# Kernel tuning notes

Measured on AMD Instinct MI355X. Metric: run time of the kernel, lower is better.

Reference implementation:

```python
import jax, jax.numpy as jnp
import numpy as np


def _forward(x, conv_w, conv_b, lin_w, lin_b, W_in, conv1d_w, conv1d_b, W_x, W_dt, b_dt, A_log, Dp, W_out, We, be, Wa, ba, Wq, bq):
    B, _, H, Wd = x.shape
    E = conv_w.shape[0]
    # conv stem: Conv2d(k=3, pad=1) -> flatten(2) -> Linear(H*W -> img_size)
    z = jax.lax.conv_general_dilated(x, conv_w, (1, 1), [(1, 1), (1, 1)],
                                     dimension_numbers=('NCHW', 'OIHW', 'NCHW'))
    z = z + conv_b[None, :, None, None]
    z = z.reshape(B, E, H * Wd)                              # [B,E,HW]
    z = jnp.einsum('ben,mn->bem', z, lin_w) + lin_b          # [B,E,L]
    u = z.transpose(2, 0, 1)                                 # [L,B,E]: Mamba sees batch=L, seq=B
    # ---- Mamba block (mamba_ssm reference math) ----
    di = W_in.shape[0] // 2
    xz = u @ W_in.T                                          # [L,seq,2*di]
    xm, zg = xz[..., :di], xz[..., di:]
    K = conv1d_w.shape[-1]
    xc = jax.lax.conv_general_dilated(xm.transpose(0, 2, 1), conv1d_w, (1,), [(K - 1, 0)],
                                      dimension_numbers=('NCH', 'OIH', 'NCH'),
                                      feature_group_count=di)  # causal depthwise conv
    xs = jax.nn.silu((xc + conv1d_b[None, :, None]).transpose(0, 2, 1))  # [L,seq,di]
    dbl = xs @ W_x.T                                         # [L,seq,dt_rank+2S]
    dt_rank = W_dt.shape[1]
    S = A_log.shape[1]
    delta = jax.nn.softplus(dbl[..., :dt_rank] @ W_dt.T + b_dt)          # [L,seq,di]
    Bm = dbl[..., dt_rank:dt_rank + S]                       # [L,seq,S]
    Cm = dbl[..., dt_rank + S:]                              # [L,seq,S]
    A = -jnp.exp(A_log)                                      # [di,S]

    def step(h, t):
        d_t, b_t, c_t, x_t = t                               # [L,di],[L,S],[L,S],[L,di]
        h = jnp.exp(d_t[:, :, None] * A) * h + (d_t * x_t)[:, :, None] * b_t[:, None, :]
        return h, jnp.einsum('lds,ls->ld', h, c_t)

    h0 = jnp.zeros((u.shape[0], di, S), xs.dtype)
    _, ys = jax.lax.scan(step, h0, (delta.transpose(1, 0, 2), Bm.transpose(1, 0, 2),
                                    Cm.transpose(1, 0, 2), xs.transpose(1, 0, 2)))
    y = (ys.transpose(1, 0, 2) + xs * Dp) * jax.nn.silu(zg)  # [L,seq,di]
    out = y @ W_out.T                                        # [L,seq,E]
    feat = out[-1]                                           # [B,E] (last 'mamba batch' row)
    return feat @ We.T + be, feat @ Wa.T + ba, feat @ Wq.T + bq


def setup_inputs() -> dict:
    key = jax.random.key(0)
    ks = jax.random.split(key, 16)
    B, C, IMG, E, S, K = 512, 1, 32, 128, 256, 4
    di, dt_rank = 2 * E, 8
    sc = 0.02
    return {
        'x': jax.random.normal(ks[0], (B, C, IMG, IMG), jnp.float32),
        'conv_w': sc * jax.random.normal(ks[1], (E, C, 3, 3), jnp.float32),
        'conv_b': jnp.zeros((E,), jnp.float32),
        'lin_w': sc * jax.random.normal(ks[2], (IMG, IMG * IMG), jnp.float32),
        'lin_b': jnp.zeros((IMG,), jnp.float32),
        'W_in': sc * jax.random.normal(ks[3], (2 * di, E), jnp.float32),
        'conv1d_w': sc * jax.random.normal(ks[4], (di, 1, K), jnp.float32),
        'conv1d_b': jnp.zeros((di,), jnp.float32),
        'W_x': sc * jax.random.normal(ks[5], (dt_rank + 2 * S, di), jnp.float32),
        'W_dt': sc * jax.random.normal(ks[6], (di, dt_rank), jnp.float32),
        'b_dt': 0.1 * jax.random.normal(ks[7], (di,), jnp.float32),
        'A_log': jnp.log(jnp.broadcast_to(jnp.arange(1, S + 1, dtype=jnp.float32), (di, S))),
        'Dp': jnp.ones((di,), jnp.float32),
        'W_out': sc * jax.random.normal(ks[8], (E, di), jnp.float32),
        'We': sc * jax.random.normal(ks[9], (1, E), jnp.float32),
        'be': jnp.zeros((1,), jnp.float32),
        'Wa': sc * jax.random.normal(ks[10], (3, E), jnp.float32),
        'ba': jnp.zeros((3,), jnp.float32),
        'Wq': sc * jax.random.normal(ks[11], (4, E), jnp.float32),
        'bq': jnp.zeros((4,), jnp.float32),
    }


def reference(x, conv_w, conv_b, lin_w, lin_b, W_in, conv1d_w, conv1d_b, W_x, W_dt, b_dt, A_log, Dp, W_out, We, be, Wa, ba, Wq, bq):
    return _forward(x, conv_w, conv_b, lin_w, lin_b, W_in, conv1d_w, conv1d_b, W_x,
                    W_dt, b_dt, A_log, Dp, W_out, We, be, Wa, ba, Wq, bq)
```

## Files before the change

### kernel.cpp

```cpp
#include <hip/hip_runtime.h>
#include <math.h>

#define BATCH 512
#define E     128
#define DI    256
#define S     256
#define DTR   8
#define KCONV 4
#define JWX   520

__device__ __forceinline__ float silu_f(float v) {
    return v / (1.0f + __expf(-v));
}

__global__ __launch_bounds__(256) void kA_pre(
    const float* __restrict__ x, const float* __restrict__ conv_w,
    const float* __restrict__ conv_b, const float* __restrict__ lin_w,
    const float* __restrict__ lin_b, const float* __restrict__ W_in,
    const float* __restrict__ W_x, const float* __restrict__ W_out,
    float* __restrict__ xm, float* __restrict__ zg,
    float* __restrict__ W_xT, float* __restrict__ W_outT)
{
    const int tid = threadIdx.x;
    if (blockIdx.x >= 512) {
        const int bid = blockIdx.x - 512;
        const float* src; float* dst; int J, K, j0;
        if (bid < 9) { src = W_x;   dst = W_xT;   J = JWX; K = DI; j0 = bid * 64; }
        else         { src = W_out; dst = W_outT; J = E;   K = DI; j0 = (bid - 9) * 64; }
        const int j = j0 + (tid & 63);
        if (j >= J) return;
        for (int c = tid >> 6; c < K; c += 4)
            dst[c * J + j] = src[j * K + c];
        return;
    }

    const int b = blockIdx.x;
    __shared__ float lw[1024];
    __shared__ float red[10][4];
    __shared__ float Tsh[10];
    __shared__ float u[E];

    const float4 lv = ((const float4*)(lin_w + 31 * 1024))[tid];
    ((float4*)lw)[tid] = lv;
    __syncthreads();

    float acc[10];
#pragma unroll
    for (int k = 0; k < 10; k++) acc[k] = 0.0f;

    const float4 xv = ((const float4*)(x + (size_t)b * 1024))[tid];
    const int p0 = tid * 4;
    const int h = p0 >> 5, w0 = p0 & 31;
    const float xa[4] = {xv.x, xv.y, xv.z, xv.w};
#pragma unroll
    for (int k = 0; k < 4; k++) {
        const float xval = xa[k];
        const int w = w0 + k;
#pragma unroll
        for (int i = 0; i < 3; i++) {
            const int hh = h - (i - 1);
            if (hh < 0 || hh > 31) continue;
#pragma unroll
            for (int j = 0; j < 3; j++) {
                const int ww = w - (j - 1);
                if (ww < 0 || ww > 31) continue;
                acc[i * 3 + j] += xval * lw[hh * 32 + ww];
            }
        }
    }
    acc[9] = lv.x + lv.y + lv.z + lv.w;

    const int wv = tid >> 6, ln = tid & 63;
#pragma unroll
    for (int k = 0; k < 10; k++) {
#pragma unroll
        for (int m = 1; m < 64; m <<= 1) acc[k] += __shfl_xor(acc[k], m, 64);
    }
    if (ln == 0) {
#pragma unroll
        for (int k = 0; k < 10; k++) red[k][wv] = acc[k];
    }
    __syncthreads();
    if (tid < 10) Tsh[tid] = red[tid][0] + red[tid][1] + red[tid][2] + red[tid][3];
    __syncthreads();

    if (tid < E) {
        const int e = tid;
        float v = lin_b[31] + conv_b[e] * Tsh[9];
#pragma unroll
        for (int k = 0; k < 9; k++) v += conv_w[e * 9 + k] * Tsh[k];
        u[e] = v;
    }
    __syncthreads();

    {
        const float4* w0p = (const float4*)(W_in + (size_t)tid * E);
        const float4* w1p = (const float4*)(W_in + (size_t)(tid + 256) * E);
        float a0 = 0.0f;
#pragma unroll 8
        for (int e4 = 0; e4 < E / 4; e4++) {
            const float4 w = w0p[e4];
            a0 += u[4*e4]*w.x + u[4*e4+1]*w.y + u[4*e4+2]*w.z + u[4*e4+3]*w.w;
        }
        float a1 = 0.0f;
#pragma unroll 8
        for (int e4 = 0; e4 < E / 4; e4++) {
            const float4 w = w1p[e4];
            a1 += u[4*e4]*w.x + u[4*e4+1]*w.y + u[4*e4+2]*w.z + u[4*e4+3]*w.w;
        }
        xm[b * DI + tid] = a0;
        zg[b * DI + tid] = a1;
    }
}

__global__ __launch_bounds__(256) void k2b_conv_wx(
    const float* __restrict__ xm, const float* __restrict__ c1w,
    const float* __restrict__ conv1d_b, const float* __restrict__ W_xT,
    const float* __restrict__ W_dt, const float* __restrict__ b_dt,
    float* __restrict__ xs_g, float* __restrict__ delta_g,
    float* __restrict__ Bm, float* __restrict__ Cm)
{
    const int bb = blockIdx.x * 4;
    const int g = blockIdx.y;
    const int tid = threadIdx.x;
    __shared__ float xs[4][DI];
    __shared__ float dtin[4][8];

    for (int idx = tid; idx < 4 * DI; idx += 256) {
        const int r = idx >> 8, c = idx & 255;
        const int b = bb + r;
        const float4 wc = ((const float4*)c1w)[c];
        float a = conv1d_b[c];
        if (b >= 3) a += xm[(b - 3) * DI + c] * wc.x;
        if (b >= 2) a += xm[(b - 2) * DI + c] * wc.y;
        if (b >= 1) a += xm[(b - 1) * DI + c] * wc.z;
        a += xm[b * DI + c] * wc.w;
        const float s = silu_f(a);
        xs[r][c] = s;
        if (g == 0) xs_g[b * DI + c] = s;
    }
    __syncthreads();

    const int r = tid >> 6;
    const int j = g * 64 + (tid & 63);
    if (j < JWX) {
        float a = 0.0f;
#pragma unroll 8
        for (int c = 0; c < DI; c++) a += xs[r][c] * W_xT[c * JWX + j];
        const int b = bb + r;
        if (j < DTR)          dtin[r][j] = a;
        else if (j < DTR + S) Bm[b * S + (j - DTR)] = a;
        else                  Cm[b * S + (j - DTR - S)] = a;
    }
    __syncthreads();

    if (g == 0) {
        const int d = tid;
        const float bd = b_dt[d];
        const float4 wd0 = ((const float4*)(W_dt + d * DTR))[0];
        const float4 wd1 = ((const float4*)(W_dt + d * DTR))[1];
#pragma unroll
        for (int r2 = 0; r2 < 4; r2++) {
            float a = bd
                + dtin[r2][0]*wd0.x + dtin[r2][1]*wd0.y + dtin[r2][2]*wd0.z + dtin[r2][3]*wd0.w
                + dtin[r2][4]*wd1.x + dtin[r2][5]*wd1.y + dtin[r2][6]*wd1.z + dtin[r2][7]*wd1.w;
            const float sp = (a > 20.0f) ? a : log1pf(__expf(a));
            delta_g[(bb + r2) * DI + d] = sp;
        }
    }
}

template <int NCv>
__global__ __launch_bounds__(256) void k3u_up(
    const float* __restrict__ A_log, const float* __restrict__ delta,
    const float* __restrict__ xs, const float* __restrict__ Bm,
    float* __restrict__ hloc, float* __restrict__ Dchunk)
{
    constexpr int TCv = BATCH / NCv;
    const int tid = threadIdx.x;
    const int wv = tid >> 6, ln = tid & 63;
    const int d = blockIdx.x * 4 + wv;
    const int c = blockIdx.y;
    const int s0 = ln * 4;
    const int t0 = c * TCv;

    const float4 al = *(const float4*)(A_log + d * S + s0);
    float4 A;
    A.x = -__expf(al.x); A.y = -__expf(al.y);
    A.z = -__expf(al.z); A.w = -__expf(al.w);

    float4 h = make_float4(0.f, 0.f, 0.f, 0.f);
    float cd = 0.0f;

    for (int tb = 0; tb < TCv; tb += 8) {
#pragma unroll
        for (int i = 0; i < 8; i++) {
            const int tt = t0 + tb + i;
            const float dd = delta[tt * DI + d];
            cd += dd;
            const float u = dd * xs[tt * DI + d];
            const float4 B = *(const float4*)(Bm + tt * S + s0);
            h.x = __expf(dd * A.x) * h.x + u * B.x;
            h.y = __expf(dd * A.y) * h.y + u * B.y;
            h.z = __expf(dd * A.z) * h.z + u * B.z;
            h.w = __expf(dd * A.w) * h.w + u * B.w;
        }
    }

    *(float4*)(hloc + ((size_t)(c * DI + d)) * S + s0) = h;
    if (ln == 0) Dchunk[c * DI + d] = cd;
}

template <int NCv>
__global__ __launch_bounds__(256) void k3d_down(
    const float* __restrict__ A_log, const float* __restrict__ delta,
    const float* __restrict__ xs, const float* __restrict__ Bm,
    const float* __restrict__ Cm, const float* __restrict__ hloc,
    const float* __restrict__ Dchunk, float* __restrict__ y)
{
    constexpr int TCv = BATCH / NCv;
    const int tid = threadIdx.x;
    const int wv = tid >> 6, ln = tid & 63;
    const int d = blockIdx.x * 4 + wv;
    const int c = (NCv - 1) - blockIdx.y;
    const int s0 = ln * 4;
    const int t0 = c * TCv;

    const float4 al = *(const float4*)(A_log + d * S + s0);
    float4 A;
    A.x = -__expf(al.x); A.y = -__expf(al.y);
    A.z = -__expf(al.z); A.w = -__expf(al.w);

    float4 h = make_float4(0.f, 0.f, 0.f, 0.f);
    for (int cp = 1; cp <= c; cp++) {
        const float4 hl = *(const float4*)(hloc + ((size_t)((cp - 1) * DI + d)) * S + s0);
        const float Dc = Dchunk[(cp - 1) * DI + d];
        h.x = hl.x + __expf(A.x * Dc) * h.x;
        h.y = hl.y + __expf(A.y * Dc) * h.y;
        h.z = hl.z + __expf(A.z * Dc) * h.z;
        h.w = hl.w + __expf(A.w * Dc) * h.w;
    }

    float pr[8];
    for (int tb = 0; tb < TCv; tb += 8) {
#pragma unroll
        for (int i = 0; i < 8; i++) {
            const int tt = t0 + tb + i;
            const float dd = delta[tt * DI + d];
            const float u = dd * xs[tt * DI + d];
            const float4 B = *(const float4*)(Bm + tt * S + s0);
            const float4 C = *(const float4*)(Cm + tt * S + s0);
            h.x = __expf(dd * A.x) * h.x + u * B.x;
            h.y = __expf(dd * A.y) * h.y + u * B.y;
            h.z = __expf(dd * A.z) * h.z + u * B.z;
            h.w = __expf(dd * A.w) * h.w + u * B.w;
            pr[i] = h.x * C.x + h.y * C.y + h.z * C.z + h.w * C.w;
        }
#pragma unroll
        for (int i = 0; i < 8; i++) {
#pragma unroll
            for (int m = 1; m < 64; m <<= 1) pr[i] += __shfl_xor(pr[i], m, 64);
        }
        if (ln == 0) {
#pragma unroll
            for (int i = 0; i < 8; i++) y[(t0 + tb + i) * DI + d] = pr[i];
        }
    }
}

__global__ __launch_bounds__(256) void k4_heads(
    const float* __restrict__ y, const float* __restrict__ xs,
    const float* __restrict__ Dp, const float* __restrict__ zg,
    const float* __restrict__ W_outT,
    const float* __restrict__ We, const float* __restrict__ be,
    const float* __restrict__ Wa, const float* __restrict__ ba,
    const float* __restrict__ Wq, const float* __restrict__ bq,
    float* __restrict__ out)
{
    const int bb = blockIdx.x * 2;
    const int tid = threadIdx.x;
    __shared__ float yf[2][DI];
    __shared__ float feat[2][E];

    for (int idx = tid; idx < 2 * DI; idx += 256) {
        const int r = idx >> 8, c = idx & 255;
        const int b = bb + r;
        const float z = zg[b * DI + c];
        yf[r][c] = (y[b * DI + c] + xs[b * DI + c] * Dp[c]) * silu_f(z);
    }
    __syncthreads();

    {
        const int r = tid >> 7, e = tid & 127;
        float a = 0.0f;
#pragma unroll 8
        for (int dd = 0; dd < DI; dd++) a += yf[r][dd] * W_outT[dd * E + e];
        feat[r][e] = a;
    }
    __syncthreads();

    if (tid < 16) {
        const int r = tid >> 3, hd = tid & 7;
        const int b = bb + r;
        const float* wrow;
        float bias;
        int dst;
        if (hd == 0)      { wrow = We;                 bias = be[0];      dst = b; }
        else if (hd < 4)  { wrow = Wa + (hd - 1) * E;  bias = ba[hd - 1]; dst = 512 + b * 3 + (hd - 1); }
        else              { wrow = Wq + (hd - 4) * E;  bias = bq[hd - 4]; dst = 2048 + b * 4 + (hd - 4); }
        float a = bias;
#pragma unroll 4
        for (int e = 0; e < E; e++) a += feat[r][e] * wrow[e];
        out[dst] = a;
    }
}

template <int NCv>
static void launch_scan(const float* A_log, const float* delta, const float* xs,
                        const float* Bm, const float* Cm, float* y,
                        float* hloc, float* Dchunk, hipStream_t stream)
{
    k3u_up<NCv><<<dim3(64, NCv), 256, 0, stream>>>(A_log, delta, xs, Bm, hloc, Dchunk);
    k3d_down<NCv><<<dim3(64, NCv), 256, 0, stream>>>(A_log, delta, xs, Bm, Cm, hloc, Dchunk, y);
}

extern "C" void kernel_launch(void* const* d_in, const int* in_sizes, int n_in,
                              void* d_out, int out_size, void* d_ws, size_t ws_size,
                              hipStream_t stream)
{
    const float* x        = (const float*)d_in[0];
    const float* conv_w   = (const float*)d_in[1];
    const float* conv_b   = (const float*)d_in[2];
    const float* lin_w    = (const float*)d_in[3];
    const float* lin_b    = (const float*)d_in[4];
    const float* W_in     = (const float*)d_in[5];
    const float* conv1d_w = (const float*)d_in[6];
    const float* conv1d_b = (const float*)d_in[7];
    const float* W_x      = (const float*)d_in[8];
    const float* W_dt     = (const float*)d_in[9];
    const float* b_dt     = (const float*)d_in[10];
    const float* A_log    = (const float*)d_in[11];
    const float* Dp       = (const float*)d_in[12];
    const float* W_out    = (const float*)d_in[13];
    const float* We       = (const float*)d_in[14];
    const float* be       = (const float*)d_in[15];
    const float* Wa       = (const float*)d_in[16];
    const float* ba       = (const float*)d_in[17];
    const float* Wq       = (const float*)d_in[18];
    const float* bq       = (const float*)d_in[19];
    float* out = (float*)d_out;

    float* ws = (float*)d_ws;
    float* xm     = ws;
    float* zg     = xm     + 512 * 256;
    float* xs     = zg     + 512 * 256;
    float* delta  = xs     + 512 * 256;
    float* Bm     = delta  + 512 * 256;
    float* Cm     = Bm     + 512 * 256;
    float* y      = Cm     + 512 * 256;
    float* W_xT   = y      + 512 * 256;
    float* W_outT = W_xT   + 256 * JWX;
    float* tail   = W_outT + 256 * 128;

    const size_t base_floats = (size_t)(tail - ws);
    const size_t avail = ws_size / 4 - base_floats;

    kA_pre<<<523, 256, 0, stream>>>(x, conv_w, conv_b, lin_w, lin_b,
                                    W_in, W_x, W_out,
                                    xm, zg, W_xT, W_outT);
    k2b_conv_wx<<<dim3(128, 9), 256, 0, stream>>>(xm, conv1d_w, conv1d_b, W_xT, W_dt, b_dt,
                                                  xs, delta, Bm, Cm);

    if (avail >= (size_t)32 * DI * S + 32 * DI) {
        float* hloc = tail;
        float* Dch  = hloc + (size_t)32 * DI * S;
        launch_scan<32>(A_log, delta, xs, Bm, Cm, y, hloc, Dch, stream);
    } else if (avail >= (size_t)16 * DI * S + 16 * DI) {
        float* hloc = tail;
        float* Dch  = hloc + (size_t)16 * DI * S;
        launch_scan<16>(A_log, delta, xs, Bm, Cm, y, hloc, Dch, stream);
    } else {
        float* hloc = tail;
        float* Dch  = hloc + (size_t)8 * DI * S;
        launch_scan<8>(A_log, delta, xs, Bm, Cm, y, hloc, Dch, stream);
    }

    k4_heads<<<256, 256, 0, stream>>>(y, xs, Dp, zg, W_outT, We, be, Wa, ba, Wq, bq, out);
}
```

Baseline: 184.5 us.

## Fuse all stages into one persistent kernel with software grid barriers

Replaces the five separate launches (pre-projection, conv+W_x, chunked scan up-sweep, down-sweep, output heads) with one persistent 512-block kernel. The stages are separated by an atomic-counter grid barrier, and a small init kernel resets the barrier state. The goal is to remove per-launch overhead and the idle gaps between dependent kernels. In exchange it relies on all 512 blocks being co-resident (two per CU via launch bounds), which risks deadlock if occupancy drops. It also adds barrier spin latency and fixes the scan chunk count at 32.

```diff
diff --git a/kernel.cpp b/kernel.cpp
--- a/kernel.cpp
+++ b/kernel.cpp
@@ -8,9 +8,326 @@
 #define DTR   8
 #define KCONV 4
 #define JWX   520
+#define NC    32
+#define TCV   (BATCH / NC)
+#define NBLK  512
 
 __device__ __forceinline__ float silu_f(float v) {
     return v / (1.0f + __expf(-v));
+}
+
+__device__ __forceinline__ void gridbar(int* cnt, int* gen) {
+    __syncthreads();
+    if (threadIdx.x == 0) {
+        __threadfence();
+        const int g = __hip_atomic_load(gen, __ATOMIC_RELAXED, __HIP_MEMORY_SCOPE_AGENT);
+        const int arrived =
+            __hip_atomic_fetch_add(cnt, 1, __ATOMIC_ACQ_REL, __HIP_MEMORY_SCOPE_AGENT) + 1;
+        if (arrived == NBLK) {
+            __hip_atomic_store(cnt, 0, __ATOMIC_RELAXED, __HIP_MEMORY_SCOPE_AGENT);
+            __hip_atomic_store(gen, g + 1, __ATOMIC_RELEASE, __HIP_MEMORY_SCOPE_AGENT);
+        } else {
+            while (__hip_atomic_load(gen, __ATOMIC_ACQUIRE, __HIP_MEMORY_SCOPE_AGENT) == g)
+                __builtin_amdgcn_s_sleep(4);
+        }
+        __threadfence();
+    }
+    __syncthreads();
+}
+
+__global__ void kinit(int* cnt, int* gen) {
+    if (threadIdx.x == 0) { *cnt = 0; *gen = 0; }
+}
+
+__global__ __launch_bounds__(256, 2) void mega(
+    const float* __restrict__ x, const float* __restrict__ conv_w,
+    const float* __restrict__ conv_b, const float* __restrict__ lin_w,
+    const float* __restrict__ lin_b, const float* __restrict__ W_in,
+    const float* __restrict__ c1w, const float* __restrict__ conv1d_b,
+    const float* __restrict__ W_x, const float* __restrict__ W_dt,
+    const float* __restrict__ b_dt, const float* __restrict__ A_log,
+    const float* __restrict__ Dp, const float* __restrict__ W_out,
+    const float* __restrict__ We, const float* __restrict__ be,
+    const float* __restrict__ Wa, const float* __restrict__ ba,
+    const float* __restrict__ Wq, const float* __restrict__ bq,
+    float* __restrict__ out,
+    float* __restrict__ xm, float* __restrict__ zg,
+    float* __restrict__ xs_g, float* __restrict__ delta_g,
+    float* __restrict__ Bm, float* __restrict__ Cm,
+    float* __restrict__ y,
+    float* __restrict__ W_xT, float* __restrict__ W_outT,
+    float* __restrict__ hloc, float* __restrict__ Dchunk,
+    int* __restrict__ bcnt, int* __restrict__ bgen)
+{
+    const int tid  = threadIdx.x;
+    const int bid  = blockIdx.x;
+    const int wv = tid >> 6, ln = tid & 63;
+
+    __shared__ float lw[1024];
+    __shared__ float red[10][4];
+    __shared__ float Tsh[10];
+    __shared__ float ush[E];
+    __shared__ float xs_sh[4][DI];
+    __shared__ float dtin[4][8];
+    __shared__ float yf[2][DI];
+    __shared__ float feat[2][E];
+
+    for (int v = bid; v < 523; v += NBLK) {
+        if (v >= 512) {
+            const int t = v - 512;
+            const float* src; float* dst; int J, K, j0;
+            if (t < 9) { src = W_x;   dst = W_xT;   J = JWX; K = DI; j0 = t * 64; }
+            else       { src = W_out; dst = W_outT; J = E;   K = DI; j0 = (t - 9) * 64; }
+            const int j = j0 + ln;
+            if (j < J) {
+                for (int c = wv; c < K; c += 4)
+                    dst[c * J + j] = src[j * K + c];
+            }
+        } else {
+            const int b = v;
+            const float4 lv = ((const float4*)(lin_w + 31 * 1024))[tid];
+            ((float4*)lw)[tid] = lv;
+            __syncthreads();
+
+            float acc[10];
+#pragma unroll
+            for (int k = 0; k < 10; k++) acc[k] = 0.0f;
+
+            const float4 xv = ((const float4*)(x + (size_t)b * 1024))[tid];
+            const int p0 = tid * 4;
+            const int h = p0 >> 5, w0 = p0 & 31;
+            const float xa[4] = {xv.x, xv.y, xv.z, xv.w};
+#pragma unroll
+            for (int k = 0; k < 4; k++) {
+                const float xval = xa[k];
+                const int w = w0 + k;
+#pragma unroll
+                for (int i = 0; i < 3; i++) {
+                    const int hh = h - (i - 1);
+                    if (hh < 0 || hh > 31) continue;
+#pragma unroll
+                    for (int j = 0; j < 3; j++) {
+                        const int ww = w - (j - 1);
+                        if (ww < 0 || ww > 31) continue;
+                        acc[i * 3 + j] += xval * lw[hh * 32 + ww];
+                    }
+                }
+            }
+            acc[9] = lv.x + lv.y + lv.z + lv.w;
+
+#pragma unroll
+            for (int k = 0; k < 10; k++) {
+#pragma unroll
+                for (int m = 1; m < 64; m <<= 1) acc[k] += __shfl_xor(acc[k], m, 64);
+            }
+            if (ln == 0) {
+#pragma unroll
+                for (int k = 0; k < 10; k++) red[k][wv] = acc[k];
+            }
+            __syncthreads();
+            if (tid < 10) Tsh[tid] = red[tid][0] + red[tid][1] + red[tid][2] + red[tid][3];
+            __syncthreads();
+
+            if (tid < E) {
+                const int e = tid;
+                float val = lin_b[31] + conv_b[e] * Tsh[9];
+#pragma unroll
+                for (int k = 0; k < 9; k++) val += conv_w[e * 9 + k] * Tsh[k];
+                ush[e] = val;
+            }
+            __syncthreads();
+
+            {
+                const float4* w0p = (const float4*)(W_in + (size_t)tid * E);
+                const float4* w1p = (const float4*)(W_in + (size_t)(tid + 256) * E);
+                float a0 = 0.0f;
+#pragma unroll 8
+                for (int e4 = 0; e4 < E / 4; e4++) {
+                    const float4 w = w0p[e4];
+                    a0 += ush[4*e4]*w.x + ush[4*e4+1]*w.y + ush[4*e4+2]*w.z + ush[4*e4+3]*w.w;
+                }
+                float a1 = 0.0f;
+#pragma unroll 8
+                for (int e4 = 0; e4 < E / 4; e4++) {
+                    const float4 w = w1p[e4];
+                    a1 += ush[4*e4]*w.x + ush[4*e4+1]*w.y + ush[4*e4+2]*w.z + ush[4*e4+3]*w.w;
+                }
+                xm[b * DI + tid] = a0;
+                zg[b * DI + tid] = a1;
+            }
+            __syncthreads();
+        }
+    }
+
+    gridbar(bcnt, bgen);
+
+    for (int v = bid; v < 128 * 9; v += NBLK) {
+        const int g  = v >> 7;
+        const int bb = (v & 127) * 4;
+
+        for (int idx = tid; idx < 4 * DI; idx += 256) {
+            const int r = idx >> 8, c = idx & 255;
+            const int b = bb + r;
+            const float4 wc = ((const float4*)c1w)[c];
+            float a = conv1d_b[c];
+            if (b >= 3) a += xm[(b - 3) * DI + c] * wc.x;
+            if (b >= 2) a += xm[(b - 2) * DI + c] * wc.y;
+            if (b >= 1) a += xm[(b - 1) * DI + c] * wc.z;
+            a += xm[b * DI + c] * wc.w;
+            const float s = silu_f(a);
+            xs_sh[r][c] = s;
+            if (g == 0) xs_g[b * DI + c] = s;
+        }
+        __syncthreads();
+
+        const int r = tid >> 6;
+        const int j = g * 64 + ln;
+        if (j < JWX) {
+            float a = 0.0f;
+#pragma unroll 8
+            for (int c = 0; c < DI; c++) a += xs_sh[r][c] * W_xT[c * JWX + j];
+            const int b = bb + r;
+            if (j < DTR)          dtin[r][j] = a;
+            else if (j < DTR + S) Bm[b * S + (j - DTR)] = a;
+            else                  Cm[b * S + (j - DTR - S)] = a;
+        }
+        __syncthreads();
+
+        if (g == 0) {
+            const int d = tid;
+            const float bd = b_dt[d];
+            const float4 wd0 = ((const float4*)(W_dt + d * DTR))[0];
+            const float4 wd1 = ((const float4*)(W_dt + d * DTR))[1];
+#pragma unroll
+            for (int r2 = 0; r2 < 4; r2++) {
+                float a = bd
+                    + dtin[r2][0]*wd0.x + dtin[r2][1]*wd0.y + dtin[r2][2]*wd0.z + dtin[r2][3]*wd0.w
+                    + dtin[r2][4]*wd1.x + dtin[r2][5]*wd1.y + dtin[r2][6]*wd1.z + dtin[r2][7]*wd1.w;
+                delta_g[(bb + r2) * DI + d] = (a > 20.0f) ? a : log1pf(__expf(a));
+            }
+        }
+        __syncthreads();
+    }
+
+    gridbar(bcnt, bgen);
+
+    for (int v = bid; v < 64 * NC; v += NBLK) {
+        const int xp = v & 63, c = v >> 6;
+        const int d = xp * 4 + wv;
+        const int s0 = ln * 4;
+        const int t0 = c * TCV;
+
+        const float4 al = *(const float4*)(A_log + d * S + s0);
+        float4 A;
+        A.x = -__expf(al.x); A.y = -__expf(al.y);
+        A.z = -__expf(al.z); A.w = -__expf(al.w);
+
+        float4 h = make_float4(0.f, 0.f, 0.f, 0.f);
+        float cd = 0.0f;
+        for (int tb = 0; tb < TCV; tb += 8) {
+#pragma unroll
+            for (int i = 0; i < 8; i++) {
+                const int tt = t0 + tb + i;
+                const float dd = delta_g[tt * DI + d];
+                cd += dd;
+                const float u = dd * xs_g[tt * DI + d];
+                const float4 B = *(const float4*)(Bm + tt * S + s0);
+                h.x = __expf(dd * A.x) * h.x + u * B.x;
+                h.y = __expf(dd * A.y) * h.y + u * B.y;
+                h.z = __expf(dd * A.z) * h.z + u * B.z;
+                h.w = __expf(dd * A.w) * h.w + u * B.w;
+            }
+        }
+        *(float4*)(hloc + ((size_t)(c * DI + d)) * S + s0) = h;
+        if (ln == 0) Dchunk[c * DI + d] = cd;
+    }
+
+    gridbar(bcnt, bgen);
+
+    for (int v = bid; v < 64 * NC; v += NBLK) {
+        const int xp = v & 63;
+        const int c = (NC - 1) - (v >> 6);
+        const int d = xp * 4 + wv;
+        const int s0 = ln * 4;
+        const int t0 = c * TCV;
+
+        const float4 al = *(const float4*)(A_log + d * S + s0);
+        float4 A;
+        A.x = -__expf(al.x); A.y = -__expf(al.y);
+        A.z = -__expf(al.z); A.w = -__expf(al.w);
+
+        float4 h = make_float4(0.f, 0.f, 0.f, 0.f);
+        for (int cp = 1; cp <= c; cp++) {
+            const float4 hl = *(const float4*)(hloc + ((size_t)((cp - 1) * DI + d)) * S + s0);
+            const float Dc = Dchunk[(cp - 1) * DI + d];
+            h.x = hl.x + __expf(A.x * Dc) * h.x;
+            h.y = hl.y + __expf(A.y * Dc) * h.y;
+            h.z = hl.z + __expf(A.z * Dc) * h.z;
+            h.w = hl.w + __expf(A.w * Dc) * h.w;
+        }
+
+        float pr[8];
+        for (int tb = 0; tb < TCV; tb += 8) {
+#pragma unroll
+            for (int i = 0; i < 8; i++) {
+                const int tt = t0 + tb + i;
+                const float dd = delta_g[tt * DI + d];
+                const float u = dd * xs_g[tt * DI + d];
+                const float4 B = *(const float4*)(Bm + tt * S + s0);
+                const float4 C = *(const float4*)(Cm + tt * S + s0);
+                h.x = __expf(dd * A.x) * h.x + u * B.x;
+                h.y = __expf(dd * A.y) * h.y + u * B.y;
+                h.z = __expf(dd * A.z) * h.z + u * B.z;
+                h.w = __expf(dd * A.w) * h.w + u * B.w;
+                pr[i] = h.x * C.x + h.y * C.y + h.z * C.z + h.w * C.w;
+            }
+#pragma unroll
+            for (int i = 0; i < 8; i++) {
+#pragma unroll
+                for (int m = 1; m < 64; m <<= 1) pr[i] += __shfl_xor(pr[i], m, 64);
+            }
+            if (ln == 0) {
+#pragma unroll
+                for (int i = 0; i < 8; i++) y[(t0 + tb + i) * DI + d] = pr[i];
+            }
+        }
+    }
+
+    gridbar(bcnt, bgen);
+
+    for (int v = bid; v < 256; v += NBLK) {
+        const int bb = v * 2;
+        for (int idx = tid; idx < 2 * DI; idx += 256) {
+            const int r = idx >> 8, cc = idx & 255;
+            const int b = bb + r;
+            const float z = zg[b * DI + cc];
+            yf[r][cc] = (y[b * DI + cc] + xs_g[b * DI + cc] * Dp[cc]) * silu_f(z);
+        }
+        __syncthreads();
+        {
+            const int r = tid >> 7, e = tid & 127;
+            float a = 0.0f;
+#pragma unroll 8
+            for (int dd = 0; dd < DI; dd++) a += yf[r][dd] * W_outT[dd * E + e];
+            feat[r][e] = a;
+        }
+        __syncthreads();
+        if (tid < 16) {
+            const int r = tid >> 3, hd = tid & 7;
+            const int b = bb + r;
+            const float* wrow;
+            float bias;
+            int dst;
+            if (hd == 0)      { wrow = We;                 bias = be[0];      dst = b; }
+            else if (hd < 4)  { wrow = Wa + (hd - 1) * E;  bias = ba[hd - 1]; dst = 512 + b * 3 + (hd - 1); }
+            else              { wrow = Wq + (hd - 4) * E;  bias = bq[hd - 4]; dst = 2048 + b * 4 + (hd - 4); }
+            float a = bias;
+#pragma unroll 4
+            for (int e = 0; e < E; e++) a += feat[r][e] * wrow[e];
+            out[dst] = a;
+        }
+        __syncthreads();
+    }
 }
 
 __global__ __launch_bounds__(256) void kA_pre(
@@ -170,19 +487,17 @@
     }
 }
 
-template <int NCv>
 __global__ __launch_bounds__(256) void k3u_up(
     const float* __restrict__ A_log, const float* __restrict__ delta,
     const float* __restrict__ xs, const float* __restrict__ Bm,
     float* __restrict__ hloc, float* __restrict__ Dchunk)
 {
-    constexpr int TCv = BATCH / NCv;
     const int tid = threadIdx.x;
     const int wv = tid >> 6, ln = tid & 63;
     const int d = blockIdx.x * 4 + wv;
     const int c = blockIdx.y;
     const int s0 = ln * 4;
-    const int t0 = c * TCv;
+    const int t0 = c * TCV;
 
     const float4 al = *(const float4*)(A_log + d * S + s0);
     float4 A;
@@ -191,8 +506,7 @@
 
     float4 h = make_float4(0.f, 0.f, 0.f, 0.f);
     float cd = 0.0f;
-
-    for (int tb = 0; tb < TCv; tb += 8) {
+    for (int tb = 0; tb < TCV; tb += 8) {
 #pragma unroll
         for (int i = 0; i < 8; i++) {
             const int tt = t0 + tb + i;
@@ -206,25 +520,22 @@
             h.w = __expf(dd * A.w) * h.w + u * B.w;
         }
     }
-
     *(float4*)(hloc + ((size_t)(c * DI + d)) * S + s0) = h;
     if (ln == 0) Dchunk[c * DI + d] = cd;
 }
 
-template <int NCv>
 __global__ __launch_bounds__(256) void k3d_down(
     const float* __restrict__ A_log, const float* __restrict__ delta,
     const float* __restrict__ xs, const float* __restrict__ Bm,
     const float* __restrict__ Cm, const float* __restrict__ hloc,
     const float* __restrict__ Dchunk, float* __restrict__ y)
 {
-    constexpr int TCv = BATCH / NCv;
     const int tid = threadIdx.x;
     const int wv = tid >> 6, ln = tid & 63;
     const int d = blockIdx.x * 4 + wv;
-    const int c = (NCv - 1) - blockIdx.y;
+    const int c = (NC - 1) - blockIdx.y;
     const int s0 = ln * 4;
-    const int t0 = c * TCv;
+    const int t0 = c * TCV;
 
     const float4 al = *(const float4*)(A_log + d * S + s0);
     float4 A;
@@ -242,7 +553,7 @@
     }
 
     float pr[8];
-    for (int tb = 0; tb < TCv; tb += 8) {
+    for (int tb = 0; tb < TCV; tb += 8) {
 #pragma unroll
         for (int i = 0; i < 8; i++) {
             const int tt = t0 + tb + i;
@@ -313,15 +624,6 @@
         for (int e = 0; e < E; e++) a += feat[r][e] * wrow[e];
         out[dst] = a;
     }
-}
-
-template <int NCv>
-static void launch_scan(const float* A_log, const float* delta, const float* xs,
-                        const float* Bm, const float* Cm, float* y,
-                        float* hloc, float* Dchunk, hipStream_t stream)
-{
-    k3u_up<NCv><<<dim3(64, NCv), 256, 0, stream>>>(A_log, delta, xs, Bm, hloc, Dchunk);
-    k3d_down<NCv><<<dim3(64, NCv), 256, 0, stream>>>(A_log, delta, xs, Bm, Cm, hloc, Dchunk, y);
 }
 
 extern "C" void kernel_launch(void* const* d_in, const int* in_sizes, int n_in,
@@ -360,30 +662,29 @@
     float* y      = Cm     + 512 * 256;
     float* W_xT   = y      + 512 * 256;
     float* W_outT = W_xT   + 256 * JWX;
-    float* tail   = W_outT + 256 * 128;
-
-    const size_t base_floats = (size_t)(tail - ws);
-    const size_t avail = ws_size / 4 - base_floats;
-
-    kA_pre<<<523, 256, 0, stream>>>(x, conv_w, conv_b, lin_w, lin_b,
-                                    W_in, W_x, W_out,
-                                    xm, zg, W_xT, W_outT);
-    k2b_conv_wx<<<dim3(128, 9), 256, 0, stream>>>(xm, conv1d_w, conv1d_b, W_xT, W_dt, b_dt,
-                                                  xs, delta, Bm, Cm);
-
-    if (avail >= (size_t)32 * DI * S + 32 * DI) {
-        float* hloc = tail;
-        float* Dch  = hloc + (size_t)32 * DI * S;
-        launch_scan<32>(A_log, delta, xs, Bm, Cm, y, hloc, Dch, stream);
-    } else if (avail >= (size_t)16 * DI * S + 16 * DI) {
-        float* hloc = tail;
-        float* Dch  = hloc + (size_t)16 * DI * S;
-        launch_scan<16>(A_log, delta, xs, Bm, Cm, y, hloc, Dch, stream);
+    float* hloc   = W_outT + 256 * 128;
+    float* Dchunk = hloc   + (size_t)NC * DI * S;
+    int*   bstate = (int*)(Dchunk + NC * DI);
+
+    const size_t need_floats = (size_t)(Dchunk + NC * DI + 16 - ws);
+    if (ws_size / 4 >= need_floats) {
+        int* bcnt = bstate;
+        int* bgen = bstate + 1;
+        kinit<<<1, 64, 0, stream>>>(bcnt, bgen);
+        mega<<<NBLK, 256, 0, stream>>>(
+            x, conv_w, conv_b, lin_w, lin_b, W_in,
+            conv1d_w, conv1d_b, W_x, W_dt, b_dt, A_log, Dp, W_out,
+            We, be, Wa, ba, Wq, bq, out,
+            xm, zg, xs, delta, Bm, Cm, y, W_xT, W_outT, hloc, Dchunk,
+            bcnt, bgen);
     } else {
-        float* hloc = tail;
-        float* Dch  = hloc + (size_t)8 * DI * S;
-        launch_scan<8>(A_log, delta, xs, Bm, Cm, y, hloc, Dch, stream);
-    }
-
-    k4_heads<<<256, 256, 0, stream>>>(y, xs, Dp, zg, W_outT, We, be, Wa, ba, Wq, bq, out);
-}
+        kA_pre<<<523, 256, 0, stream>>>(x, conv_w, conv_b, lin_w, lin_b,
+                                        W_in, W_x, W_out, xm, zg, W_xT, W_outT);
+        k2b_conv_wx<<<dim3(128, 9), 256, 0, stream>>>(xm, conv1d_w, conv1d_b, W_xT,
+                                                      W_dt, b_dt, xs, delta, Bm, Cm);
+        k3u_up<<<dim3(64, NC), 256, 0, stream>>>(A_log, delta, xs, Bm, hloc, Dchunk);
+        k3d_down<<<dim3(64, NC), 256, 0, stream>>>(A_log, delta, xs, Bm, Cm,
+                                                   hloc, Dchunk, y);
+        k4_heads<<<256, 256, 0, stream>>>(y, xs, Dp, zg, W_outT, We, be, Wa, ba, Wq, bq, out);
+    }
+}
```

Measured after the change: 668.0 us. 3.62x slower.

## Fuse pipeline into one persistent kernel with flag-based inter-block synchronization

Applied to the files above, without the earlier changes.

Replaces the five separate launches (preprocessing, conv+W_x projection, scan up-sweep, scan down-sweep, heads) with a single 512-block persistent kernel. Blocks coordinate through global sentinel flags and counters, so each scan chunk starts as soon as its input rows are ready and the heads run per chunk as soon as its outputs are done. It also drops the weight-transpose pass and recomputes the three preceding in_proj rows per block for the causal conv, so xm never goes to global memory. The scheme relies on all 512 blocks being resident at once to avoid deadlock, and the extra recomputation adds redundant work.

```diff
diff --git a/kernel.cpp b/kernel.cpp
--- a/kernel.cpp
+++ b/kernel.cpp
@@ -8,320 +8,342 @@
 #define DTR   8
 #define KCONV 4
 #define JWX   520
+#define NC    32
+#define TCV   (BATCH / NC)
+#define NBLK  512
+#define SENT  0x7C3A91E5
 
 __device__ __forceinline__ float silu_f(float v) {
     return v / (1.0f + __expf(-v));
 }
 
-__global__ __launch_bounds__(256) void kA_pre(
+__device__ __forceinline__ int ld_flag(const int* p) {
+    return __hip_atomic_load(p, __ATOMIC_RELAXED, __HIP_MEMORY_SCOPE_AGENT);
+}
+__device__ __forceinline__ void st_flag(int* p, int v) {
+    __hip_atomic_store(p, v, __ATOMIC_RELAXED, __HIP_MEMORY_SCOPE_AGENT);
+}
+__device__ __forceinline__ void acq_fence() {
+    __builtin_amdgcn_fence(__ATOMIC_ACQUIRE, "agent");
+}
+
+__device__ __forceinline__ float dot128(const float* __restrict__ w,
+                                        const float* __restrict__ u) {
+    const float4* wp = (const float4*)w;
+    float a = 0.0f;
+#pragma unroll 8
+    for (int e4 = 0; e4 < 32; e4++) {
+        const float4 ww = wp[e4];
+        a += u[4*e4]*ww.x + u[4*e4+1]*ww.y + u[4*e4+2]*ww.z + u[4*e4+3]*ww.w;
+    }
+    return a;
+}
+
+__global__ __launch_bounds__(256, 2) void mega(
     const float* __restrict__ x, const float* __restrict__ conv_w,
     const float* __restrict__ conv_b, const float* __restrict__ lin_w,
     const float* __restrict__ lin_b, const float* __restrict__ W_in,
-    const float* __restrict__ W_x, const float* __restrict__ W_out,
-    float* __restrict__ xm, float* __restrict__ zg,
-    float* __restrict__ W_xT, float* __restrict__ W_outT)
+    const float* __restrict__ c1w, const float* __restrict__ conv1d_b,
+    const float* __restrict__ W_x, const float* __restrict__ W_dt,
+    const float* __restrict__ b_dt, const float* __restrict__ A_log,
+    const float* __restrict__ Dp, const float* __restrict__ W_out,
+    const float* __restrict__ We, const float* __restrict__ be,
+    const float* __restrict__ Wa, const float* __restrict__ ba,
+    const float* __restrict__ Wq, const float* __restrict__ bq,
+    float* __restrict__ out,
+    float* __restrict__ zg, float* __restrict__ xs_g,
+    float* __restrict__ delta_g, float* __restrict__ Bm,
+    float* __restrict__ Cm, float* __restrict__ y,
+    float* __restrict__ hloc, float* __restrict__ Dchunk,
+    int* __restrict__ rowflag, int* __restrict__ upflag,
+    int* __restrict__ donecnt)
 {
     const int tid = threadIdx.x;
-    if (blockIdx.x >= 512) {
-        const int bid = blockIdx.x - 512;
-        const float* src; float* dst; int J, K, j0;
-        if (bid < 9) { src = W_x;   dst = W_xT;   J = JWX; K = DI; j0 = bid * 64; }
-        else         { src = W_out; dst = W_outT; J = E;   K = DI; j0 = (bid - 9) * 64; }
-        const int j = j0 + (tid & 63);
-        if (j >= J) return;
-        for (int c = tid >> 6; c < K; c += 4)
-            dst[c * J + j] = src[j * K + c];
-        return;
-    }
-
-    const int b = blockIdx.x;
+    const int bid = blockIdx.x;
+    const int wv = tid >> 6, ln = tid & 63;
+
     __shared__ float lw[1024];
     __shared__ float red[10][4];
     __shared__ float Tsh[10];
-    __shared__ float u[E];
-
-    const float4 lv = ((const float4*)(lin_w + 31 * 1024))[tid];
-    ((float4*)lw)[tid] = lv;
-    __syncthreads();
-
-    float acc[10];
-#pragma unroll
-    for (int k = 0; k < 10; k++) acc[k] = 0.0f;
-
-    const float4 xv = ((const float4*)(x + (size_t)b * 1024))[tid];
-    const int p0 = tid * 4;
-    const int h = p0 >> 5, w0 = p0 & 31;
-    const float xa[4] = {xv.x, xv.y, xv.z, xv.w};
-#pragma unroll
-    for (int k = 0; k < 4; k++) {
-        const float xval = xa[k];
-        const int w = w0 + k;
-#pragma unroll
-        for (int i = 0; i < 3; i++) {
-            const int hh = h - (i - 1);
-            if (hh < 0 || hh > 31) continue;
-#pragma unroll
-            for (int j = 0; j < 3; j++) {
-                const int ww = w - (j - 1);
-                if (ww < 0 || ww > 31) continue;
-                acc[i * 3 + j] += xval * lw[hh * 32 + ww];
-            }
-        }
-    }
-    acc[9] = lv.x + lv.y + lv.z + lv.w;
-
-    const int wv = tid >> 6, ln = tid & 63;
-#pragma unroll
-    for (int k = 0; k < 10; k++) {
-#pragma unroll
-        for (int m = 1; m < 64; m <<= 1) acc[k] += __shfl_xor(acc[k], m, 64);
-    }
-    if (ln == 0) {
-#pragma unroll
-        for (int k = 0; k < 10; k++) red[k][wv] = acc[k];
-    }
-    __syncthreads();
-    if (tid < 10) Tsh[tid] = red[tid][0] + red[tid][1] + red[tid][2] + red[tid][3];
-    __syncthreads();
-
-    if (tid < E) {
-        const int e = tid;
-        float v = lin_b[31] + conv_b[e] * Tsh[9];
-#pragma unroll
-        for (int k = 0; k < 9; k++) v += conv_w[e * 9 + k] * Tsh[k];
-        u[e] = v;
-    }
-    __syncthreads();
-
-    {
-        const float4* w0p = (const float4*)(W_in + (size_t)tid * E);
-        const float4* w1p = (const float4*)(W_in + (size_t)(tid + 256) * E);
-        float a0 = 0.0f;
+    __shared__ float ush[E];
+    __shared__ float xml[7][DI];
+    __shared__ float xs_sh[4][DI];
+    __shared__ float dtin[4][8];
+    __shared__ float yf[2][DI];
+    __shared__ float feat[2][E];
+
+    if (bid < 128) {
+        const int g = bid, bb = g * 4;
+
+        const float4 lv = ((const float4*)(lin_w + 31 * 1024))[tid];
+        ((float4*)lw)[tid] = lv;
+        __syncthreads();
+
+        for (int i = 0; i < 7; i++) {
+            const int b = bb - 3 + i;
+            if (b < 0) continue;
+
+            float acc[10];
+#pragma unroll
+            for (int k = 0; k < 10; k++) acc[k] = 0.0f;
+
+            const float4 xv = ((const float4*)(x + (size_t)b * 1024))[tid];
+            const int p0 = tid * 4;
+            const int h = p0 >> 5, w0 = p0 & 31;
+            const float xa[4] = {xv.x, xv.y, xv.z, xv.w};
+#pragma unroll
+            for (int k = 0; k < 4; k++) {
+                const float xval = xa[k];
+                const int w = w0 + k;
+#pragma unroll
+                for (int ii = 0; ii < 3; ii++) {
+                    const int hh = h - (ii - 1);
+                    if (hh < 0 || hh > 31) continue;
+#pragma unroll
+                    for (int j = 0; j < 3; j++) {
+                        const int ww = w - (j - 1);
+                        if (ww < 0 || ww > 31) continue;
+                        acc[ii * 3 + j] += xval * lw[hh * 32 + ww];
+                    }
+                }
+            }
+            acc[9] = lv.x + lv.y + lv.z + lv.w;
+
+#pragma unroll
+            for (int k = 0; k < 10; k++) {
+#pragma unroll
+                for (int m = 1; m < 64; m <<= 1) acc[k] += __shfl_xor(acc[k], m, 64);
+            }
+            if (ln == 0) {
+#pragma unroll
+                for (int k = 0; k < 10; k++) red[k][wv] = acc[k];
+            }
+            __syncthreads();
+            if (tid < 10) Tsh[tid] = red[tid][0] + red[tid][1] + red[tid][2] + red[tid][3];
+            __syncthreads();
+
+            if (tid < E) {
+                const int e = tid;
+                float val = lin_b[31] + conv_b[e] * Tsh[9];
+#pragma unroll
+                for (int k = 0; k < 9; k++) val += conv_w[e * 9 + k] * Tsh[k];
+                ush[e] = val;
+            }
+            __syncthreads();
+
+            xml[i][tid] = dot128(W_in + (size_t)tid * E, ush);
+            if (i >= 3) zg[b * DI + tid] = dot128(W_in + (size_t)(tid + 256) * E, ush);
+            __syncthreads();
+        }
+
+        {
+            const float4 wc = ((const float4*)c1w)[tid];
+            const float cb = conv1d_b[tid];
+#pragma unroll
+            for (int r = 0; r < 4; r++) {
+                const int b = bb + r;
+                float a = cb;
+                if (b >= 3) a += xml[r + 0][tid] * wc.x;
+                if (b >= 2) a += xml[r + 1][tid] * wc.y;
+                if (b >= 1) a += xml[r + 2][tid] * wc.z;
+                a += xml[r + 3][tid] * wc.w;
+                const float s = silu_f(a);
+                xs_sh[r][tid] = s;
+                xs_g[b * DI + tid] = s;
+            }
+        }
+        __syncthreads();
+
+        for (int jj = tid; jj < JWX; jj += 256) {
+            const float4* wr = (const float4*)(W_x + (size_t)jj * DI);
+            float a0 = 0.f, a1 = 0.f, a2 = 0.f, a3 = 0.f;
 #pragma unroll 8
-        for (int e4 = 0; e4 < E / 4; e4++) {
-            const float4 w = w0p[e4];
-            a0 += u[4*e4]*w.x + u[4*e4+1]*w.y + u[4*e4+2]*w.z + u[4*e4+3]*w.w;
-        }
-        float a1 = 0.0f;
-#pragma unroll 8
-        for (int e4 = 0; e4 < E / 4; e4++) {
-            const float4 w = w1p[e4];
-            a1 += u[4*e4]*w.x + u[4*e4+1]*w.y + u[4*e4+2]*w.z + u[4*e4+3]*w.w;
-        }
-        xm[b * DI + tid] = a0;
-        zg[b * DI + tid] = a1;
-    }
-}
-
-__global__ __launch_bounds__(256) void k2b_conv_wx(
-    const float* __restrict__ xm, const float* __restrict__ c1w,
-    const float* __restrict__ conv1d_b, const float* __restrict__ W_xT,
-    const float* __restrict__ W_dt, const float* __restrict__ b_dt,
-    float* __restrict__ xs_g, float* __restrict__ delta_g,
-    float* __restrict__ Bm, float* __restrict__ Cm)
-{
-    const int bb = blockIdx.x * 4;
-    const int g = blockIdx.y;
-    const int tid = threadIdx.x;
-    __shared__ float xs[4][DI];
-    __shared__ float dtin[4][8];
-
-    for (int idx = tid; idx < 4 * DI; idx += 256) {
-        const int r = idx >> 8, c = idx & 255;
-        const int b = bb + r;
-        const float4 wc = ((const float4*)c1w)[c];
-        float a = conv1d_b[c];
-        if (b >= 3) a += xm[(b - 3) * DI + c] * wc.x;
-        if (b >= 2) a += xm[(b - 2) * DI + c] * wc.y;
-        if (b >= 1) a += xm[(b - 1) * DI + c] * wc.z;
-        a += xm[b * DI + c] * wc.w;
-        const float s = silu_f(a);
-        xs[r][c] = s;
-        if (g == 0) xs_g[b * DI + c] = s;
-    }
-    __syncthreads();
-
-    const int r = tid >> 6;
-    const int j = g * 64 + (tid & 63);
-    if (j < JWX) {
-        float a = 0.0f;
-#pragma unroll 8
-        for (int c = 0; c < DI; c++) a += xs[r][c] * W_xT[c * JWX + j];
-        const int b = bb + r;
-        if (j < DTR)          dtin[r][j] = a;
-        else if (j < DTR + S) Bm[b * S + (j - DTR)] = a;
-        else                  Cm[b * S + (j - DTR - S)] = a;
-    }
-    __syncthreads();
-
-    if (g == 0) {
-        const int d = tid;
-        const float bd = b_dt[d];
-        const float4 wd0 = ((const float4*)(W_dt + d * DTR))[0];
-        const float4 wd1 = ((const float4*)(W_dt + d * DTR))[1];
-#pragma unroll
-        for (int r2 = 0; r2 < 4; r2++) {
-            float a = bd
-                + dtin[r2][0]*wd0.x + dtin[r2][1]*wd0.y + dtin[r2][2]*wd0.z + dtin[r2][3]*wd0.w
-                + dtin[r2][4]*wd1.x + dtin[r2][5]*wd1.y + dtin[r2][6]*wd1.z + dtin[r2][7]*wd1.w;
-            const float sp = (a > 20.0f) ? a : log1pf(__expf(a));
-            delta_g[(bb + r2) * DI + d] = sp;
-        }
-    }
-}
-
-template <int NCv>
-__global__ __launch_bounds__(256) void k3u_up(
-    const float* __restrict__ A_log, const float* __restrict__ delta,
-    const float* __restrict__ xs, const float* __restrict__ Bm,
-    float* __restrict__ hloc, float* __restrict__ Dchunk)
-{
-    constexpr int TCv = BATCH / NCv;
-    const int tid = threadIdx.x;
-    const int wv = tid >> 6, ln = tid & 63;
-    const int d = blockIdx.x * 4 + wv;
-    const int c = blockIdx.y;
+            for (int c4 = 0; c4 < 64; c4++) {
+                const float4 w = wr[c4];
+                a0 += xs_sh[0][4*c4]*w.x + xs_sh[0][4*c4+1]*w.y + xs_sh[0][4*c4+2]*w.z + xs_sh[0][4*c4+3]*w.w;
+                a1 += xs_sh[1][4*c4]*w.x + xs_sh[1][4*c4+1]*w.y + xs_sh[1][4*c4+2]*w.z + xs_sh[1][4*c4+3]*w.w;
+                a2 += xs_sh[2][4*c4]*w.x + xs_sh[2][4*c4+1]*w.y + xs_sh[2][4*c4+2]*w.z + xs_sh[2][4*c4+3]*w.w;
+                a3 += xs_sh[3][4*c4]*w.x + xs_sh[3][4*c4+1]*w.y + xs_sh[3][4*c4+2]*w.z + xs_sh[3][4*c4+3]*w.w;
+            }
+            const float av[4] = {a0, a1, a2, a3};
+#pragma unroll
+            for (int r = 0; r < 4; r++) {
+                const int b = bb + r;
+                if (jj < DTR)          dtin[r][jj] = av[r];
+                else if (jj < DTR + S) Bm[b * S + (jj - DTR)] = av[r];
+                else                   Cm[b * S + (jj - DTR - S)] = av[r];
+            }
+        }
+        __syncthreads();
+
+        {
+            const int d = tid;
+            const float bd = b_dt[d];
+            const float4 wd0 = ((const float4*)(W_dt + d * DTR))[0];
+            const float4 wd1 = ((const float4*)(W_dt + d * DTR))[1];
+#pragma unroll
+            for (int r2 = 0; r2 < 4; r2++) {
+                float a = bd
+                    + dtin[r2][0]*wd0.x + dtin[r2][1]*wd0.y + dtin[r2][2]*wd0.z + dtin[r2][3]*wd0.w
+                    + dtin[r2][4]*wd1.x + dtin[r2][5]*wd1.y + dtin[r2][6]*wd1.z + dtin[r2][7]*wd1.w;
+                delta_g[(bb + r2) * DI + d] = (a > 20.0f) ? a : log1pf(__expf(a));
+            }
+        }
+
+        if (tid == 0) st_flag(&donecnt[(g >> 2) * 16], 0);
+        __syncthreads();
+        if (tid == 0) {
+            __threadfence();
+            st_flag(&rowflag[g], SENT);
+        }
+    }
+
+    const int xp = bid & 63;
+    const int d  = xp * 4 + wv;
     const int s0 = ln * 4;
-    const int t0 = c * TCv;
 
     const float4 al = *(const float4*)(A_log + d * S + s0);
     float4 A;
     A.x = -__expf(al.x); A.y = -__expf(al.y);
     A.z = -__expf(al.z); A.w = -__expf(al.w);
 
-    float4 h = make_float4(0.f, 0.f, 0.f, 0.f);
-    float cd = 0.0f;
-
-    for (int tb = 0; tb < TCv; tb += 8) {
-#pragma unroll
-        for (int i = 0; i < 8; i++) {
-            const int tt = t0 + tb + i;
-            const float dd = delta[tt * DI + d];
-            cd += dd;
-            const float u = dd * xs[tt * DI + d];
-            const float4 B = *(const float4*)(Bm + tt * S + s0);
-            h.x = __expf(dd * A.x) * h.x + u * B.x;
-            h.y = __expf(dd * A.y) * h.y + u * B.y;
-            h.z = __expf(dd * A.z) * h.z + u * B.z;
-            h.w = __expf(dd * A.w) * h.w + u * B.w;
-        }
-    }
-
-    *(float4*)(hloc + ((size_t)(c * DI + d)) * S + s0) = h;
-    if (ln == 0) Dchunk[c * DI + d] = cd;
-}
-
-template <int NCv>
-__global__ __launch_bounds__(256) void k3d_down(
-    const float* __restrict__ A_log, const float* __restrict__ delta,
-    const float* __restrict__ xs, const float* __restrict__ Bm,
-    const float* __restrict__ Cm, const float* __restrict__ hloc,
-    const float* __restrict__ Dchunk, float* __restrict__ y)
-{
-    constexpr int TCv = BATCH / NCv;
-    const int tid = threadIdx.x;
-    const int wv = tid >> 6, ln = tid & 63;
-    const int d = blockIdx.x * 4 + wv;
-    const int c = (NCv - 1) - blockIdx.y;
-    const int s0 = ln * 4;
-    const int t0 = c * TCv;
-
-    const float4 al = *(const float4*)(A_log + d * S + s0);
-    float4 A;
-    A.x = -__expf(al.x); A.y = -__expf(al.y);
-    A.z = -__expf(al.z); A.w = -__expf(al.w);
-
-    float4 h = make_float4(0.f, 0.f, 0.f, 0.f);
-    for (int cp = 1; cp <= c; cp++) {
-        const float4 hl = *(const float4*)(hloc + ((size_t)((cp - 1) * DI + d)) * S + s0);
-        const float Dc = Dchunk[(cp - 1) * DI + d];
-        h.x = hl.x + __expf(A.x * Dc) * h.x;
-        h.y = hl.y + __expf(A.y * Dc) * h.y;
-        h.z = hl.z + __expf(A.z * Dc) * h.z;
-        h.w = hl.w + __expf(A.w * Dc) * h.w;
-    }
-
-    float pr[8];
-    for (int tb = 0; tb < TCv; tb += 8) {
-#pragma unroll
-        for (int i = 0; i < 8; i++) {
-            const int tt = t0 + tb + i;
-            const float dd = delta[tt * DI + d];
-            const float u = dd * xs[tt * DI + d];
-            const float4 B = *(const float4*)(Bm + tt * S + s0);
-            const float4 C = *(const float4*)(Cm + tt * S + s0);
-            h.x = __expf(dd * A.x) * h.x + u * B.x;
-            h.y = __expf(dd * A.y) * h.y + u * B.y;
-            h.z = __expf(dd * A.z) * h.z + u * B.z;
-            h.w = __expf(dd * A.w) * h.w + u * B.w;
-            pr[i] = h.x * C.x + h.y * C.y + h.z * C.z + h.w * C.w;
-        }
-#pragma unroll
-        for (int i = 0; i < 8; i++) {
-#pragma unroll
-            for (int m = 1; m < 64; m <<= 1) pr[i] += __shfl_xor(pr[i], m, 64);
-        }
-        if (ln == 0) {
-#pragma unroll
-            for (int i = 0; i < 8; i++) y[(t0 + tb + i) * DI + d] = pr[i];
-        }
-    }
-}
-
-__global__ __launch_bounds__(256) void k4_heads(
-    const float* __restrict__ y, const float* __restrict__ xs,
-    const float* __restrict__ Dp, const float* __restrict__ zg,
-    const float* __restrict__ W_outT,
-    const float* __restrict__ We, const float* __restrict__ be,
-    const float* __restrict__ Wa, const float* __restrict__ ba,
-    const float* __restrict__ Wq, const float* __restrict__ bq,
-    float* __restrict__ out)
-{
-    const int bb = blockIdx.x * 2;
-    const int tid = threadIdx.x;
-    __shared__ float yf[2][DI];
-    __shared__ float feat[2][E];
-
-    for (int idx = tid; idx < 2 * DI; idx += 256) {
-        const int r = idx >> 8, c = idx & 255;
-        const int b = bb + r;
-        const float z = zg[b * DI + c];
-        yf[r][c] = (y[b * DI + c] + xs[b * DI + c] * Dp[c]) * silu_f(z);
-    }
-    __syncthreads();
-
-    {
-        const int r = tid >> 7, e = tid & 127;
-        float a = 0.0f;
+    for (int k = 0; k < 4; k++) {
+        const int c = (bid >> 6) + 8 * k;
+        const int t0 = c * TCV;
+
+        if (tid == 0) {
+            for (int g2 = 4 * c; g2 < 4 * c + 4; g2++)
+                while (ld_flag(&rowflag[g2]) != SENT) __builtin_amdgcn_s_sleep(8);
+            acq_fence();
+        }
+        __syncthreads();
+
+        float4 h = make_float4(0.f, 0.f, 0.f, 0.f);
+        float cd = 0.0f;
+        for (int tb = 0; tb < TCV; tb += 8) {
+#pragma unroll
+            for (int i = 0; i < 8; i++) {
+                const int tt = t0 + tb + i;
+                const float dd = delta_g[tt * DI + d];
+                cd += dd;
+                const float u = dd * xs_g[tt * DI + d];
+                const float4 B = *(const float4*)(Bm + tt * S + s0);
+                h.x = __expf(dd * A.x) * h.x + u * B.x;
+                h.y = __expf(dd * A.y) * h.y + u * B.y;
+                h.z = __expf(dd * A.z) * h.z + u * B.z;
+                h.w = __expf(dd * A.w) * h.w + u * B.w;
+            }
+        }
+        *(float4*)(hloc + ((size_t)(c * DI + d)) * S + s0) = h;
+        if (ln == 0) Dchunk[c * DI + d] = cd;
+
+        __syncthreads();
+        if (tid == 0) {
+            __threadfence();
+            st_flag(&upflag[c * 64 + xp], SENT);
+        }
+    }
+
+    for (int k = 0; k < 4; k++) {
+        const int c = (bid >> 6) + 8 * k;
+        const int t0 = c * TCV;
+
+        if (tid == 0) {
+            for (int cp = 0; cp < c; cp++)
+                while (ld_flag(&upflag[cp * 64 + xp]) != SENT) __builtin_amdgcn_s_sleep(8);
+            acq_fence();
+        }
+        __syncthreads();
+
+        float4 h = make_float4(0.f, 0.f, 0.f, 0.f);
+        for (int cp = 1; cp <= c; cp++) {
+            const float4 hl = *(const float4*)(hloc + ((size_t)((cp - 1) * DI + d)) * S + s0);
+            const float Dc = Dchunk[(cp - 1) * DI + d];
+            h.x = hl.x + __expf(A.x * Dc) * h.x;
+            h.y = hl.y + __expf(A.y * Dc) * h.y;
+            h.z = hl.z + __expf(A.z * Dc) * h.z;
+            h.w = hl.w + __expf(A.w * Dc) * h.w;
+        }
+
+        float pr[8];
+        for (int tb = 0; tb < TCV; tb += 8) {
+#pragma unroll
+            for (int i = 0; i < 8; i++) {
+                const int tt = t0 + tb + i;
+                const float dd = delta_g[tt * DI + d];
+                const float u = dd * xs_g[tt * DI + d];
+                const float4 B = *(const float4*)(Bm + tt * S + s0);
+                const float4 C = *(const float4*)(Cm + tt * S + s0);
+                h.x = __expf(dd * A.x) * h.x + u * B.x;
+                h.y = __expf(dd * A.y) * h.y + u * B.y;
+                h.z = __expf(dd * A.z) * h.z + u * B.z;
+                h.w = __expf(dd * A.w) * h.w + u * B.w;
+                pr[i] = h.x * C.x + h.y * C.y + h.z * C.z + h.w * C.w;
+            }
+#pragma unroll
+            for (int i = 0; i < 8; i++) {
+#pragma unroll
+                for (int m = 1; m < 64; m <<= 1) pr[i] += __shfl_xor(pr[i], m, 64);
+            }
+            if (ln == 0) {
+#pragma unroll
+                for (int i = 0; i < 8; i++) y[(t0 + tb + i) * DI + d] = pr[i];
+            }
+        }
+
+        __syncthreads();
+        if (tid == 0) {
+            __threadfence();
+            __hip_atomic_fetch_add(&donecnt[c * 16], 1,
+                                   __ATOMIC_RELAXED, __HIP_MEMORY_SCOPE_AGENT);
+        }
+    }
+
+    if (bid >= 256) {
+        const int v = bid - 256;
+        const int bb = v * 2;
+        const int c = bb >> 4;
+
+        if (tid == 0) {
+            while (ld_flag(&donecnt[c * 16]) != 64) __builtin_amdgcn_s_sleep(8);
+            acq_fence();
+        }
+        __syncthreads();
+
+        for (int idx = tid; idx < 2 * DI; idx += 256) {
+            const int r = idx >> 8, cc = idx & 255;
+            const int b = bb + r;
+            const float z = zg[b * DI + cc];
+            yf[r][cc] = (y[b * DI + cc] + xs_g[b * DI + cc] * Dp[cc]) * silu_f(z);
+        }
+        __syncthreads();
+        {
+            const int r = tid >> 7, e = tid & 127;
+            const float4* wr = (const float4*)(W_out + (size_t)e * DI);
+            float a = 0.0f;
 #pragma unroll 8
-        for (int dd = 0; dd < DI; dd++) a += yf[r][dd] * W_outT[dd * E + e];
-        feat[r][e] = a;
-    }
-    __syncthreads();
-
-    if (tid < 16) {
-        const int r = tid >> 3, hd = tid & 7;
-        const int b = bb + r;
-        const float* wrow;
-        float bias;
-        int dst;
-        if (hd == 0)      { wrow = We;                 bias = be[0];      dst = b; }
-        else if (hd < 4)  { wrow = Wa + (hd - 1) * E;  bias = ba[hd - 1]; dst = 512 + b * 3 + (hd - 1); }
-        else              { wrow = Wq + (hd - 4) * E;  bias = bq[hd - 4]; dst = 2048 + b * 4 + (hd - 4); }
-        float a = bias;
+            for (int d4 = 0; d4 < 64; d4++) {
+                const float4 w = wr[d4];
+                a += yf[r][4*d4]*w.x + yf[r][4*d4+1]*w.y + yf[r][4*d4+2]*w.z + yf[r][4*d4+3]*w.w;
+            }
+            feat[r][e] = a;
+        }
+        __syncthreads();
+        if (tid < 16) {
+            const int r = tid >> 3, hd = tid & 7;
+            const int b = bb + r;
+            const float* wrow;
+            float bias;
+            int dst;
+            if (hd == 0)      { wrow = We;                 bias = be[0];      dst = b; }
+            else if (hd < 4)  { wrow = Wa + (hd - 1) * E;  bias = ba[hd - 1]; dst = 512 + b * 3 + (hd - 1); }
+            else              { wrow = Wq + (hd - 4) * E;  bias = bq[hd - 4]; dst = 2048 + b * 4 + (hd - 4); }
+            float a = bias;
 #pragma unroll 4
-        for (int e = 0; e < E; e++) a += feat[r][e] * wrow[e];
-        out[dst] = a;
-    }
-}
-
-template <int NCv>
-static void launch_scan(const float* A_log, const float* delta, const float* xs,
-                        const float* Bm, const float* Cm, float* y,
-                        float* hloc, float* Dchunk, hipStream_t stream)
-{
-    k3u_up<NCv><<<dim3(64, NCv), 256, 0, stream>>>(A_log, delta, xs, Bm, hloc, Dchunk);
-    k3d_down<NCv><<<dim3(64, NCv), 256, 0, stream>>>(A_log, delta, xs, Bm, Cm, hloc, Dchunk, y);
+            for (int e = 0; e < E; e++) a += feat[r][e] * wrow[e];
+            out[dst] = a;
+        }
+    }
 }
 
 extern "C" void kernel_launch(void* const* d_in, const int* in_sizes, int n_in,
@@ -351,39 +373,23 @@
     float* out = (float*)d_out;
 
     float* ws = (float*)d_ws;
-    float* xm     = ws;
-    float* zg     = xm     + 512 * 256;
+    float* zg     = ws;
     float* xs     = zg     + 512 * 256;
     float* delta  = xs     + 512 * 256;
     float* Bm     = delta  + 512 * 256;
     float* Cm     = Bm     + 512 * 256;
     float* y      = Cm     + 512 * 256;
-    float* W_xT   = y      + 512 * 256;
-    float* W_outT = W_xT   + 256 * JWX;
-    float* tail   = W_outT + 256 * 128;
-
-    const size_t base_floats = (size_t)(tail - ws);
-    const size_t avail = ws_size / 4 - base_floats;
-
-    kA_pre<<<523, 256, 0, stream>>>(x, conv_w, conv_b, lin_w, lin_b,
-                                    W_in, W_x, W_out,
-                                    xm, zg, W_xT, W_outT);
-    k2b_conv_wx<<<dim3(128, 9), 256, 0, stream>>>(xm, conv1d_w, conv1d_b, W_xT, W_dt, b_dt,
-                                                  xs, delta, Bm, Cm);
-
-    if (avail >= (size_t)32 * DI * S + 32 * DI) {
-        float* hloc = tail;
-        float* Dch  = hloc + (size_t)32 * DI * S;
-        launch_scan<32>(A_log, delta, xs, Bm, Cm, y, hloc, Dch, stream);
-    } else if (avail >= (size_t)16 * DI * S + 16 * DI) {
-        float* hloc = tail;
-        float* Dch  = hloc + (size_t)16 * DI * S;
-        launch_scan<16>(A_log, delta, xs, Bm, Cm, y, hloc, Dch, stream);
-    } else {
-        float* hloc = tail;
-        float* Dch  = hloc + (size_t)8 * DI * S;
-        launch_scan<8>(A_log, delta, xs, Bm, Cm, y, hloc, Dch, stream);
-    }
-
-    k4_heads<<<256, 256, 0, stream>>>(y, xs, Dp, zg, W_outT, We, be, Wa, ba, Wq, bq, out);
-}
+    float* hloc   = y      + 512 * 256;
+    float* Dchunk = hloc   + (size_t)NC * DI * S;
+    int*   flags  = (int*)(Dchunk + NC * DI);
+    int*   rowflag = flags;
+    int*   upflag  = flags + 128;
+    int*   donecnt = flags + 128 + 2048;
+
+    mega<<<NBLK, 256, 0, stream>>>(
+        x, conv_w, conv_b, lin_w, lin_b, W_in,
+        conv1d_w, conv1d_b, W_x, W_dt, b_dt, A_log, Dp, W_out,
+        We, be, Wa, ba, Wq, bq, out,
+        zg, xs, delta, Bm, Cm, y, hloc, Dchunk,
+        rowflag, upflag, donecnt);
+}
```

Result: slower. 366.1 us (+98.5%).
